# Kernel optimization log

Hardware: AMD Instinct MI355X
Metric: run time of the kernel (lower is better)

The kernel has to match this reference:

```python
import jax, jax.numpy as jnp
import numpy as np

B, R, DIM = 4096, 64, 128


def setup_inputs() -> dict:
    key = jax.random.key(0)
    ks = jax.random.split(key, 8)
    return {
        "query_emb": jax.random.normal(ks[0], (B, DIM), jnp.float32),
        "offset_emb": jax.random.normal(ks[1], (B, DIM), jnp.float32),
        "refer_embs": jax.random.normal(ks[2], (B, R, DIM), jnp.float32),
        "query_r": jax.random.normal(ks[3], (B, DIM), jnp.float32),
        "refer_r": jax.random.normal(ks[4], (B, R, DIM), jnp.float32),
        "start_embs": jax.random.normal(ks[5], (B, R, DIM), jnp.float32),
        # attn_layer_1: Linear(2*dim, dim); xavier-uniform-like scale
        "W1": jax.random.uniform(ks[6], (DIM, 2 * DIM), jnp.float32, -0.125, 0.125),
        "b1": jnp.zeros((DIM,), jnp.float32),
        # attn_layer_2: Linear(dim, dim)
        "W2": jax.random.uniform(ks[7], (DIM, DIM), jnp.float32, -0.125, 0.125),
        "b2": jnp.zeros((DIM,), jnp.float32),
    }


def reference(query_emb, offset_emb, refer_embs, query_r, refer_r, start_embs, W1, b1, W2, b2):
    # bias term per neighbor: [B, R, dim]
    bias = refer_embs - (start_embs + refer_r)
    # concat([refer_r, broadcast(query_r)]) @ W1.T split to avoid materializing the concat:
    # W1 = [W1_a | W1_b] over the 2*dim input axis
    W1a, W1b = W1[:, :DIM], W1[:, DIM:]
    h = jnp.einsum('brd,kd->brk', refer_r, W1a) \
        + jnp.einsum('bd,kd->bk', query_r, W1b)[:, None, :] + b1
    h = jax.nn.relu(h)  # [B, R, dim]
    attn = jnp.einsum('brk,dk->brd', h, W2) + b2  # attn_layer_2
    final_refer_emb = jnp.sum(attn * bias, axis=-2)  # [B, dim]
    final_query_emb = query_emb + final_refer_emb
    return (final_query_emb, offset_emb)
```

## Files before the change

### kernel.cpp

```cpp
#include <hip/hip_runtime.h>
#include <hip/hip_bf16.h>
#include <stdint.h>

#define BTOT 4096
#define RR   64
#define DIMD 128
#define WROW 40

typedef short s16x8 __attribute__((ext_vector_type(8)));
typedef float f32x4 __attribute__((ext_vector_type(4)));

__device__ __forceinline__ unsigned short f2bf(float x) {
  __hip_bfloat16 h = __float2bfloat16(x);
  return __builtin_bit_cast(unsigned short, h);
}
__device__ __forceinline__ float bf2f(unsigned short u) {
  unsigned int v = ((unsigned int)u) << 16;
  return __builtin_bit_cast(float, v);
}

__global__ __launch_bounds__(256) void prep_kernel(
    const float* __restrict__ W1, const float* __restrict__ b1,
    const float* __restrict__ query_r, const float* __restrict__ W2,
    const float* __restrict__ offset_emb,
    float* __restrict__ qproj, unsigned short* __restrict__ w1a_swz,
    unsigned short* __restrict__ w2_swz, float* __restrict__ out)
{
  __shared__ float w1b[128 * 132];
  __shared__ float qrs[256];
  const int tid = threadIdx.x;

  {
    const size_t ob = (size_t)blockIdx.x * 8 * DIMD + (size_t)tid * 4;
    *reinterpret_cast<float4*>(out + (size_t)BTOT * DIMD + ob) =
        *reinterpret_cast<const float4*>(offset_emb + ob);
  }
  {
    const int k = tid >> 1, d0 = (tid & 1) * 64;
    const float* src = W1 + k * 256 + 128 + d0;
    float* dst = &w1b[k * 132 + d0];
    #pragma unroll
    for (int i = 0; i < 64; i += 4)
      *reinterpret_cast<float4*>(dst + i) = *reinterpret_cast<const float4*>(src + i);
  }
  if (blockIdx.x < 2) {
    const float* Wsrc = (blockIdx.x == 0) ? W1 : W2;
    unsigned short* dstw = (blockIdx.x == 0) ? w1a_swz : w2_swz;
    const int stride = (blockIdx.x == 0) ? 256 : 128;
    for (int i = tid; i < 128 * 128; i += 256) {
      const int k = i >> 7, d = i & 127;
      dstw[k * 128 + (d ^ ((k & 7) << 3))] = f2bf(Wsrc[k * stride + d]);
    }
  }
  __syncthreads();

  const int b0 = blockIdx.x * 8;
  const int k = tid & 127, bh = tid >> 7;
  for (int p = 0; p < 4; ++p) {
    const int b = b0 + p * 2;
    qrs[tid] = query_r[(size_t)(b + bh) * DIMD + k];
    __syncthreads();
    float acc = b1[k];
    const float* qq = &qrs[bh * 128];
    const float* wr = &w1b[k * 132];
    #pragma unroll
    for (int d = 0; d < 128; d += 4) {
      float4 wv = *reinterpret_cast<const float4*>(wr + d);
      float4 qv = *reinterpret_cast<const float4*>(qq + d);
      acc = fmaf(wv.x, qv.x, acc); acc = fmaf(wv.y, qv.y, acc);
      acc = fmaf(wv.z, qv.z, acc); acc = fmaf(wv.w, qv.w, acc);
    }
    qproj[(size_t)(b + bh) * DIMD + k] = acc;
    __syncthreads();
  }
}

__global__ __launch_bounds__(512) void main_kernel(
    const float* __restrict__ query_emb,
    const float* __restrict__ refer_embs, const float* __restrict__ refer_r,
    const float* __restrict__ start_embs, const float* __restrict__ b2,
    const float* __restrict__ qproj, const unsigned short* __restrict__ w1a_swz,
    const unsigned short* __restrict__ w2_swz, float* __restrict__ out)
{
  __shared__ unsigned short lds_w1a[128 * 128];
  __shared__ unsigned short lds_w2[128 * 128];
  __shared__ unsigned short wbuf[8][16 * WROW];

  const int tid  = threadIdx.x;
  const int wave = tid >> 6;
  const int lane = tid & 63;
  const int g    = lane >> 4;
  const int c    = lane & 15;

  {
    const uint4* s1 = reinterpret_cast<const uint4*>(w1a_swz);
    const uint4* s2 = reinterpret_cast<const uint4*>(w2_swz);
    uint4* d1 = reinterpret_cast<uint4*>(lds_w1a);
    uint4* d2 = reinterpret_cast<uint4*>(lds_w2);
    #pragma unroll
    for (int i = 0; i < 4; ++i) {
      d1[tid + 512 * i] = s1[tid + 512 * i];
      d2[tid + 512 * i] = s2[tid + 512 * i];
    }
  }
  __syncthreads();

  unsigned short* mybuf = &wbuf[wave][0];
  const int srl = lane >> 2;
  const int q   = lane & 3;
  const int swc = (c & 7) << 3;
  const int rl4 = 4 * g;

  const int b = blockIdx.x * 8 + wave;

  float qn[8], b2v[8], acc[8];
  #pragma unroll
  for (int nt = 0; nt < 8; ++nt) {
    qn[nt]  = qproj[(size_t)b * DIMD + nt * 16 + c];
    b2v[nt] = b2[nt * 16 + c];
    acc[nt] = 0.f;
  }

  for (int it = 0; it < 4; ++it) {
    const size_t rowbase = ((size_t)b * RR + it * 16 + srl) * DIMD;
    uint4 bp[4];
    f32x4 Ch[8];
    #pragma unroll
    for (int nt = 0; nt < 8; ++nt) Ch[nt] = (f32x4){qn[nt], qn[nt], qn[nt], qn[nt]};

    #pragma unroll
    for (int Q = 0; Q < 4; ++Q) {
      const size_t gb = rowbase + Q * 32 + q * 8;
      const float4 rv0 = *reinterpret_cast<const float4*>(refer_r    + gb);
      const float4 rv1 = *reinterpret_cast<const float4*>(refer_r    + gb + 4);
      const float4 ev0 = *reinterpret_cast<const float4*>(refer_embs + gb);
      const float4 ev1 = *reinterpret_cast<const float4*>(refer_embs + gb + 4);
      const float4 sv0 = *reinterpret_cast<const float4*>(start_embs + gb);
      const float4 sv1 = *reinterpret_cast<const float4*>(start_embs + gb + 4);
      {
        union { unsigned short u[8]; uint4 v; } pk;
        pk.u[0] = f2bf(rv0.x); pk.u[1] = f2bf(rv0.y);
        pk.u[2] = f2bf(rv0.z); pk.u[3] = f2bf(rv0.w);
        pk.u[4] = f2bf(rv1.x); pk.u[5] = f2bf(rv1.y);
        pk.u[6] = f2bf(rv1.z); pk.u[7] = f2bf(rv1.w);
        *reinterpret_cast<uint4*>(&mybuf[srl * WROW + q * 8]) = pk.v;
      }
      {
        union { unsigned short u[8]; uint4 v; } pk;
        pk.u[0] = f2bf(ev0.x - sv0.x - rv0.x); pk.u[1] = f2bf(ev0.y - sv0.y - rv0.y);
        pk.u[2] = f2bf(ev0.z - sv0.z - rv0.z); pk.u[3] = f2bf(ev0.w - sv0.w - rv0.w);
        pk.u[4] = f2bf(ev1.x - sv1.x - rv1.x); pk.u[5] = f2bf(ev1.y - sv1.y - rv1.y);
        pk.u[6] = f2bf(ev1.z - sv1.z - rv1.z); pk.u[7] = f2bf(ev1.w - sv1.w - rv1.w);
        bp[Q] = pk.v;
      }
      asm volatile("s_waitcnt lgkmcnt(0)" ::: "memory");
      const s16x8 af = *reinterpret_cast<const s16x8*>(&mybuf[c * WROW + g * 8]);
      #pragma unroll
      for (int nt = 0; nt < 8; ++nt) {
        s16x8 wf = *reinterpret_cast<const s16x8*>(
            &lds_w1a[(nt * 16 + c) * DIMD + ((Q * 32 + g * 8) ^ swc)]);
        Ch[nt] = __builtin_amdgcn_mfma_f32_16x16x32_bf16(af, wf, Ch[nt], 0, 0, 0);
      }
      asm volatile("s_waitcnt lgkmcnt(0)" ::: "memory");
    }

    f32x4 Ca[8];
    #pragma unroll
    for (int nt = 0; nt < 8; ++nt) Ca[nt] = (f32x4){b2v[nt], b2v[nt], b2v[nt], b2v[nt]};
    #pragma unroll
    for (int Q = 0; Q < 4; ++Q) {
      #pragma unroll
      for (int ntl = 0; ntl < 2; ++ntl)
        #pragma unroll
        for (int r = 0; r < 4; ++r)
          mybuf[(rl4 + r) * WROW + ntl * 16 + c] = f2bf(fmaxf(Ch[2 * Q + ntl][r], 0.f));
      asm volatile("s_waitcnt lgkmcnt(0)" ::: "memory");
      const s16x8 hf = *reinterpret_cast<const s16x8*>(&mybuf[c * WROW + g * 8]);
      #pragma unroll
      for (int nt = 0; nt < 8; ++nt) {
        s16x8 wf = *reinterpret_cast<const s16x8*>(
            &lds_w2[(nt * 16 + c) * DIMD + ((Q * 32 + g * 8) ^ swc)]);
        Ca[nt] = __builtin_amdgcn_mfma_f32_16x16x32_bf16(hf, wf, Ca[nt], 0, 0, 0);
      }
      asm volatile("s_waitcnt lgkmcnt(0)" ::: "memory");
    }

    #pragma unroll
    for (int Q = 0; Q < 4; ++Q) {
      *reinterpret_cast<uint4*>(&mybuf[srl * WROW + q * 8]) = bp[Q];
      asm volatile("s_waitcnt lgkmcnt(0)" ::: "memory");
      #pragma unroll
      for (int ntl = 0; ntl < 2; ++ntl) {
        const int nt = 2 * Q + ntl;
        float s = 0.f;
        #pragma unroll
        for (int r = 0; r < 4; ++r) {
          const float bcv = bf2f(mybuf[(rl4 + r) * WROW + ntl * 16 + c]);
          s = fmaf(Ca[nt][r], bcv, s);
        }
        s += __shfl_xor(s, 16);
        s += __shfl_xor(s, 32);
        acc[nt] += s;
      }
      asm volatile("s_waitcnt lgkmcnt(0)" ::: "memory");
    }
  }

  if (lane < 16) {
    #pragma unroll
    for (int nt = 0; nt < 8; ++nt)
      out[(size_t)b * DIMD + nt * 16 + c] =
          query_emb[(size_t)b * DIMD + nt * 16 + c] + acc[nt];
  }
}

extern "C" void kernel_launch(void* const* d_in, const int* in_sizes, int n_in,
                              void* d_out, int out_size, void* d_ws, size_t ws_size,
                              hipStream_t stream) {
  const float* query_emb  = (const float*)d_in[0];
  const float* offset_emb = (const float*)d_in[1];
  const float* refer_embs = (const float*)d_in[2];
  const float* query_r    = (const float*)d_in[3];
  const float* refer_r    = (const float*)d_in[4];
  const float* start_embs = (const float*)d_in[5];
  const float* W1 = (const float*)d_in[6];
  const float* b1 = (const float*)d_in[7];
  const float* W2 = (const float*)d_in[8];
  const float* b2 = (const float*)d_in[9];
  float* out = (float*)d_out;

  float* qproj = (float*)d_ws;
  unsigned short* w1a_swz =
      (unsigned short*)((char*)d_ws + (size_t)BTOT * DIMD * sizeof(float));
  unsigned short* w2_swz = w1a_swz + 128 * 128;

  hipLaunchKernelGGL(prep_kernel, dim3(512), dim3(256), 0, stream,
                     W1, b1, query_r, W2, offset_emb, qproj, w1a_swz, w2_swz, out);
  hipLaunchKernelGGL(main_kernel, dim3(512), dim3(512), 0, stream,
                     query_emb, refer_embs, refer_r, start_embs,
                     b2, qproj, w1a_swz, w2_swz, out);
}
```

Baseline: 109.5 us.

## Process two batches per wave and prefetch next neighbor chunk loads

Each wave now handles two batch rows, with separate LDS staging buffers, and the grid is halved to 256 blocks. The global loads for the next 32-column chunk are issued before the current chunk's MFMAs, so memory latency overlaps with compute. The explicit s_waitcnt barriers are dropped, and LDS ordering is left to the compiler. This adds instruction-level parallelism and amortises the weight reads from LDS, at the cost of more registers and only one 8-wave block per CU, which lowers occupancy.

```diff
diff --git a/kernel.cpp b/kernel.cpp
--- a/kernel.cpp
+++ b/kernel.cpp
@@ -84,7 +84,7 @@
 {
   __shared__ unsigned short lds_w1a[128 * 128];
   __shared__ unsigned short lds_w2[128 * 128];
-  __shared__ unsigned short wbuf[8][16 * WROW];
+  __shared__ unsigned short tq[8][2][16 * WROW];
 
   const int tid  = threadIdx.x;
   const int wave = tid >> 6;
@@ -105,112 +105,158 @@
   }
   __syncthreads();
 
-  unsigned short* mybuf = &wbuf[wave][0];
   const int srl = lane >> 2;
   const int q   = lane & 3;
   const int swc = (c & 7) << 3;
   const int rl4 = 4 * g;
 
-  const int b = blockIdx.x * 8 + wave;
-
-  float qn[8], b2v[8], acc[8];
+  const int bA = blockIdx.x * 16 + wave * 2;
+  unsigned short* tch[2] = { &tq[wave][0][0], &tq[wave][1][0] };
+
+  float qn[2][8], acc[2][8], b2v[8];
   #pragma unroll
   for (int nt = 0; nt < 8; ++nt) {
-    qn[nt]  = qproj[(size_t)b * DIMD + nt * 16 + c];
     b2v[nt] = b2[nt * 16 + c];
-    acc[nt] = 0.f;
+    #pragma unroll
+    for (int j = 0; j < 2; ++j) {
+      qn[j][nt]  = qproj[(size_t)(bA + j) * DIMD + nt * 16 + c];
+      acc[j][nt] = 0.f;
+    }
   }
 
   for (int it = 0; it < 4; ++it) {
-    const size_t rowbase = ((size_t)b * RR + it * 16 + srl) * DIMD;
-    uint4 bp[4];
-    f32x4 Ch[8];
-    #pragma unroll
-    for (int nt = 0; nt < 8; ++nt) Ch[nt] = (f32x4){qn[nt], qn[nt], qn[nt], qn[nt]};
+    size_t rowbase[2];
+    #pragma unroll
+    for (int j = 0; j < 2; ++j)
+      rowbase[j] = ((size_t)(bA + j) * RR + it * 16 + srl) * DIMD;
+
+    float4 rv[2][2], ev[2][2], sv[2][2];
+    #pragma unroll
+    for (int j = 0; j < 2; ++j) {
+      const size_t gb = rowbase[j] + q * 8;
+      rv[j][0] = *reinterpret_cast<const float4*>(refer_r    + gb);
+      rv[j][1] = *reinterpret_cast<const float4*>(refer_r    + gb + 4);
+      ev[j][0] = *reinterpret_cast<const float4*>(refer_embs + gb);
+      ev[j][1] = *reinterpret_cast<const float4*>(refer_embs + gb + 4);
+      sv[j][0] = *reinterpret_cast<const float4*>(start_embs + gb);
+      sv[j][1] = *reinterpret_cast<const float4*>(start_embs + gb + 4);
+    }
+
+    uint4 bp[2][4];
+    f32x4 Ch[2][8];
+    #pragma unroll
+    for (int j = 0; j < 2; ++j)
+      #pragma unroll
+      for (int nt = 0; nt < 8; ++nt)
+        Ch[j][nt] = (f32x4){qn[j][nt], qn[j][nt], qn[j][nt], qn[j][nt]};
 
     #pragma unroll
     for (int Q = 0; Q < 4; ++Q) {
-      const size_t gb = rowbase + Q * 32 + q * 8;
-      const float4 rv0 = *reinterpret_cast<const float4*>(refer_r    + gb);
-      const float4 rv1 = *reinterpret_cast<const float4*>(refer_r    + gb + 4);
-      const float4 ev0 = *reinterpret_cast<const float4*>(refer_embs + gb);
-      const float4 ev1 = *reinterpret_cast<const float4*>(refer_embs + gb + 4);
-      const float4 sv0 = *reinterpret_cast<const float4*>(start_embs + gb);
-      const float4 sv1 = *reinterpret_cast<const float4*>(start_embs + gb + 4);
-      {
-        union { unsigned short u[8]; uint4 v; } pk;
-        pk.u[0] = f2bf(rv0.x); pk.u[1] = f2bf(rv0.y);
-        pk.u[2] = f2bf(rv0.z); pk.u[3] = f2bf(rv0.w);
-        pk.u[4] = f2bf(rv1.x); pk.u[5] = f2bf(rv1.y);
-        pk.u[6] = f2bf(rv1.z); pk.u[7] = f2bf(rv1.w);
-        *reinterpret_cast<uint4*>(&mybuf[srl * WROW + q * 8]) = pk.v;
-      }
-      {
-        union { unsigned short u[8]; uint4 v; } pk;
-        pk.u[0] = f2bf(ev0.x - sv0.x - rv0.x); pk.u[1] = f2bf(ev0.y - sv0.y - rv0.y);
-        pk.u[2] = f2bf(ev0.z - sv0.z - rv0.z); pk.u[3] = f2bf(ev0.w - sv0.w - rv0.w);
-        pk.u[4] = f2bf(ev1.x - sv1.x - rv1.x); pk.u[5] = f2bf(ev1.y - sv1.y - rv1.y);
-        pk.u[6] = f2bf(ev1.z - sv1.z - rv1.z); pk.u[7] = f2bf(ev1.w - sv1.w - rv1.w);
-        bp[Q] = pk.v;
-      }
-      asm volatile("s_waitcnt lgkmcnt(0)" ::: "memory");
-      const s16x8 af = *reinterpret_cast<const s16x8*>(&mybuf[c * WROW + g * 8]);
-      #pragma unroll
-      for (int nt = 0; nt < 8; ++nt) {
-        s16x8 wf = *reinterpret_cast<const s16x8*>(
-            &lds_w1a[(nt * 16 + c) * DIMD + ((Q * 32 + g * 8) ^ swc)]);
-        Ch[nt] = __builtin_amdgcn_mfma_f32_16x16x32_bf16(af, wf, Ch[nt], 0, 0, 0);
-      }
-      asm volatile("s_waitcnt lgkmcnt(0)" ::: "memory");
-    }
-
-    f32x4 Ca[8];
-    #pragma unroll
-    for (int nt = 0; nt < 8; ++nt) Ca[nt] = (f32x4){b2v[nt], b2v[nt], b2v[nt], b2v[nt]};
+      #pragma unroll
+      for (int j = 0; j < 2; ++j) {
+        {
+          union { unsigned short u[8]; uint4 v; } pk;
+          pk.u[0] = f2bf(rv[j][0].x); pk.u[1] = f2bf(rv[j][0].y);
+          pk.u[2] = f2bf(rv[j][0].z); pk.u[3] = f2bf(rv[j][0].w);
+          pk.u[4] = f2bf(rv[j][1].x); pk.u[5] = f2bf(rv[j][1].y);
+          pk.u[6] = f2bf(rv[j][1].z); pk.u[7] = f2bf(rv[j][1].w);
+          *reinterpret_cast<uint4*>(&tch[j][srl * WROW + q * 8]) = pk.v;
+        }
+        {
+          union { unsigned short u[8]; uint4 v; } pk;
+          pk.u[0] = f2bf(ev[j][0].x - sv[j][0].x - rv[j][0].x);
+          pk.u[1] = f2bf(ev[j][0].y - sv[j][0].y - rv[j][0].y);
+          pk.u[2] = f2bf(ev[j][0].z - sv[j][0].z - rv[j][0].z);
+          pk.u[3] = f2bf(ev[j][0].w - sv[j][0].w - rv[j][0].w);
+          pk.u[4] = f2bf(ev[j][1].x - sv[j][1].x - rv[j][1].x);
+          pk.u[5] = f2bf(ev[j][1].y - sv[j][1].y - rv[j][1].y);
+          pk.u[6] = f2bf(ev[j][1].z - sv[j][1].z - rv[j][1].z);
+          pk.u[7] = f2bf(ev[j][1].w - sv[j][1].w - rv[j][1].w);
+          bp[j][Q] = pk.v;
+        }
+      }
+      if (Q < 3) {
+        #pragma unroll
+        for (int j = 0; j < 2; ++j) {
+          const size_t gb = rowbase[j] + (Q + 1) * 32 + q * 8;
+          rv[j][0] = *reinterpret_cast<const float4*>(refer_r    + gb);
+          rv[j][1] = *reinterpret_cast<const float4*>(refer_r    + gb + 4);
+          ev[j][0] = *reinterpret_cast<const float4*>(refer_embs + gb);
+          ev[j][1] = *reinterpret_cast<const float4*>(refer_embs + gb + 4);
+          sv[j][0] = *reinterpret_cast<const float4*>(start_embs + gb);
+          sv[j][1] = *reinterpret_cast<const float4*>(start_embs + gb + 4);
+        }
+      }
+      #pragma unroll
+      for (int j = 0; j < 2; ++j) {
+        const s16x8 af = *reinterpret_cast<const s16x8*>(&tch[j][c * WROW + g * 8]);
+        #pragma unroll
+        for (int nt = 0; nt < 8; ++nt) {
+          s16x8 wf = *reinterpret_cast<const s16x8*>(
+              &lds_w1a[(nt * 16 + c) * DIMD + ((Q * 32 + g * 8) ^ swc)]);
+          Ch[j][nt] = __builtin_amdgcn_mfma_f32_16x16x32_bf16(af, wf, Ch[j][nt], 0, 0, 0);
+        }
+      }
+    }
+
+    f32x4 Ca[2][8];
+    #pragma unroll
+    for (int j = 0; j < 2; ++j)
+      #pragma unroll
+      for (int nt = 0; nt < 8; ++nt)
+        Ca[j][nt] = (f32x4){b2v[nt], b2v[nt], b2v[nt], b2v[nt]};
     #pragma unroll
     for (int Q = 0; Q < 4; ++Q) {
       #pragma unroll
-      for (int ntl = 0; ntl < 2; ++ntl)
-        #pragma unroll
-        for (int r = 0; r < 4; ++r)
-          mybuf[(rl4 + r) * WROW + ntl * 16 + c] = f2bf(fmaxf(Ch[2 * Q + ntl][r], 0.f));
-      asm volatile("s_waitcnt lgkmcnt(0)" ::: "memory");
-      const s16x8 hf = *reinterpret_cast<const s16x8*>(&mybuf[c * WROW + g * 8]);
-      #pragma unroll
-      for (int nt = 0; nt < 8; ++nt) {
-        s16x8 wf = *reinterpret_cast<const s16x8*>(
-            &lds_w2[(nt * 16 + c) * DIMD + ((Q * 32 + g * 8) ^ swc)]);
-        Ca[nt] = __builtin_amdgcn_mfma_f32_16x16x32_bf16(hf, wf, Ca[nt], 0, 0, 0);
-      }
-      asm volatile("s_waitcnt lgkmcnt(0)" ::: "memory");
+      for (int j = 0; j < 2; ++j)
+        #pragma unroll
+        for (int ntl = 0; ntl < 2; ++ntl)
+          #pragma unroll
+          for (int r = 0; r < 4; ++r)
+            tch[j][(rl4 + r) * WROW + ntl * 16 + c] =
+                f2bf(fmaxf(Ch[j][2 * Q + ntl][r], 0.f));
+      #pragma unroll
+      for (int j = 0; j < 2; ++j) {
+        const s16x8 hf = *reinterpret_cast<const s16x8*>(&tch[j][c * WROW + g * 8]);
+        #pragma unroll
+        for (int nt = 0; nt < 8; ++nt) {
+          s16x8 wf = *reinterpret_cast<const s16x8*>(
+              &lds_w2[(nt * 16 + c) * DIMD + ((Q * 32 + g * 8) ^ swc)]);
+          Ca[j][nt] = __builtin_amdgcn_mfma_f32_16x16x32_bf16(hf, wf, Ca[j][nt], 0, 0, 0);
+        }
+      }
     }
 
     #pragma unroll
     for (int Q = 0; Q < 4; ++Q) {
-      *reinterpret_cast<uint4*>(&mybuf[srl * WROW + q * 8]) = bp[Q];
-      asm volatile("s_waitcnt lgkmcnt(0)" ::: "memory");
-      #pragma unroll
-      for (int ntl = 0; ntl < 2; ++ntl) {
-        const int nt = 2 * Q + ntl;
-        float s = 0.f;
-        #pragma unroll
-        for (int r = 0; r < 4; ++r) {
-          const float bcv = bf2f(mybuf[(rl4 + r) * WROW + ntl * 16 + c]);
-          s = fmaf(Ca[nt][r], bcv, s);
-        }
-        s += __shfl_xor(s, 16);
-        s += __shfl_xor(s, 32);
-        acc[nt] += s;
-      }
-      asm volatile("s_waitcnt lgkmcnt(0)" ::: "memory");
+      #pragma unroll
+      for (int j = 0; j < 2; ++j)
+        *reinterpret_cast<uint4*>(&tch[j][srl * WROW + q * 8]) = bp[j][Q];
+      #pragma unroll
+      for (int j = 0; j < 2; ++j)
+        #pragma unroll
+        for (int ntl = 0; ntl < 2; ++ntl) {
+          const int nt = 2 * Q + ntl;
+          float s = 0.f;
+          #pragma unroll
+          for (int r = 0; r < 4; ++r) {
+            const float bcv = bf2f(tch[j][(rl4 + r) * WROW + ntl * 16 + c]);
+            s = fmaf(Ca[j][nt][r], bcv, s);
+          }
+          s += __shfl_xor(s, 16);
+          s += __shfl_xor(s, 32);
+          acc[j][nt] += s;
+        }
     }
   }
 
   if (lane < 16) {
     #pragma unroll
-    for (int nt = 0; nt < 8; ++nt)
-      out[(size_t)b * DIMD + nt * 16 + c] =
-          query_emb[(size_t)b * DIMD + nt * 16 + c] + acc[nt];
+    for (int j = 0; j < 2; ++j)
+      #pragma unroll
+      for (int nt = 0; nt < 8; ++nt)
+        out[(size_t)(bA + j) * DIMD + nt * 16 + c] =
+            query_emb[(size_t)(bA + j) * DIMD + nt * 16 + c] + acc[j][nt];
   }
 }
 
@@ -236,7 +282,7 @@
 
   hipLaunchKernelGGL(prep_kernel, dim3(512), dim3(256), 0, stream,
                      W1, b1, query_r, W2, offset_emb, qproj, w1a_swz, w2_swz, out);
-  hipLaunchKernelGGL(main_kernel, dim3(512), dim3(512), 0, stream,
+  hipLaunchKernelGGL(main_kernel, dim3(256), dim3(512), 0, stream,
                      query_emb, refer_embs, refer_r, start_embs,
                      b2, qproj, w1a_swz, w2_swz, out);
 }
```

After: 151.9 us. 1.39x slower.

## Prefetch next neighbor chunk into registers and process two batches per wave

Applied to the files above, without the earlier changes.

Each wave now handles two batch rows, and the grid shrinks to 256 blocks, so the LDS weight staging is amortized over more work. The global loads of refer_r, refer_embs and start_embs for the next 32-column chunk are issued before the current chunk's MFMAs run, forming a register double-buffer across the whole two-batch sequence. The explicit lgkmcnt waits are removed and left to the compiler. The goal is to hide HBM latency in this memory-bound kernel, at the cost of more live registers and fewer resident waves per CU.

```diff
diff --git a/kernel.cpp b/kernel.cpp
--- a/kernel.cpp
+++ b/kernel.cpp
@@ -111,107 +111,125 @@
   const int swc = (c & 7) << 3;
   const int rl4 = 4 * g;
 
-  const int b = blockIdx.x * 8 + wave;
-
-  float qn[8], b2v[8], acc[8];
+  const int bA = blockIdx.x * 16 + wave * 2;
+
+  float b2v[8];
   #pragma unroll
-  for (int nt = 0; nt < 8; ++nt) {
-    qn[nt]  = qproj[(size_t)b * DIMD + nt * 16 + c];
-    b2v[nt] = b2[nt * 16 + c];
-    acc[nt] = 0.f;
-  }
-
-  for (int it = 0; it < 4; ++it) {
-    const size_t rowbase = ((size_t)b * RR + it * 16 + srl) * DIMD;
-    uint4 bp[4];
-    f32x4 Ch[8];
-    #pragma unroll
-    for (int nt = 0; nt < 8; ++nt) Ch[nt] = (f32x4){qn[nt], qn[nt], qn[nt], qn[nt]};
-
-    #pragma unroll
-    for (int Q = 0; Q < 4; ++Q) {
-      const size_t gb = rowbase + Q * 32 + q * 8;
-      const float4 rv0 = *reinterpret_cast<const float4*>(refer_r    + gb);
-      const float4 rv1 = *reinterpret_cast<const float4*>(refer_r    + gb + 4);
-      const float4 ev0 = *reinterpret_cast<const float4*>(refer_embs + gb);
-      const float4 ev1 = *reinterpret_cast<const float4*>(refer_embs + gb + 4);
-      const float4 sv0 = *reinterpret_cast<const float4*>(start_embs + gb);
-      const float4 sv1 = *reinterpret_cast<const float4*>(start_embs + gb + 4);
-      {
-        union { unsigned short u[8]; uint4 v; } pk;
-        pk.u[0] = f2bf(rv0.x); pk.u[1] = f2bf(rv0.y);
-        pk.u[2] = f2bf(rv0.z); pk.u[3] = f2bf(rv0.w);
-        pk.u[4] = f2bf(rv1.x); pk.u[5] = f2bf(rv1.y);
-        pk.u[6] = f2bf(rv1.z); pk.u[7] = f2bf(rv1.w);
-        *reinterpret_cast<uint4*>(&mybuf[srl * WROW + q * 8]) = pk.v;
+  for (int nt = 0; nt < 8; ++nt) b2v[nt] = b2[nt * 16 + c];
+
+  float4 Prv0, Prv1, Pev0, Pev1, Psv0, Psv1;
+
+#define LOADQ(fq) do {                                                        \
+    const int bb_ = (fq) >> 4, it_ = ((fq) >> 2) & 3, Q_ = (fq) & 3;          \
+    const size_t gb_ =                                                        \
+        ((size_t)(bA + bb_) * RR + it_ * 16 + srl) * DIMD + Q_ * 32 + q * 8;  \
+    Prv0 = *reinterpret_cast<const float4*>(refer_r    + gb_);                \
+    Prv1 = *reinterpret_cast<const float4*>(refer_r    + gb_ + 4);            \
+    Pev0 = *reinterpret_cast<const float4*>(refer_embs + gb_);                \
+    Pev1 = *reinterpret_cast<const float4*>(refer_embs + gb_ + 4);            \
+    Psv0 = *reinterpret_cast<const float4*>(start_embs + gb_);                \
+    Psv1 = *reinterpret_cast<const float4*>(start_embs + gb_ + 4);            \
+  } while (0)
+
+  LOADQ(0);
+
+  #pragma unroll
+  for (int bb = 0; bb < 2; ++bb) {
+    const int b = bA + bb;
+
+    float qn[8], acc[8];
+    #pragma unroll
+    for (int nt = 0; nt < 8; ++nt) {
+      qn[nt]  = qproj[(size_t)b * DIMD + nt * 16 + c];
+      acc[nt] = 0.f;
+    }
+
+    for (int it = 0; it < 4; ++it) {
+      uint4 bp[4];
+      f32x4 Ch[8];
+      #pragma unroll
+      for (int nt = 0; nt < 8; ++nt) Ch[nt] = (f32x4){qn[nt], qn[nt], qn[nt], qn[nt]};
+
+      #pragma unroll
+      for (int Q = 0; Q < 4; ++Q) {
+        {
+          union { unsigned short u[8]; uint4 v; } pk;
+          pk.u[0] = f2bf(Prv0.x); pk.u[1] = f2bf(Prv0.y);
+          pk.u[2] = f2bf(Prv0.z); pk.u[3] = f2bf(Prv0.w);
+          pk.u[4] = f2bf(Prv1.x); pk.u[5] = f2bf(Prv1.y);
+          pk.u[6] = f2bf(Prv1.z); pk.u[7] = f2bf(Prv1.w);
+          *reinterpret_cast<uint4*>(&mybuf[srl * WROW + q * 8]) = pk.v;
+        }
+        {
+          union { unsigned short u[8]; uint4 v; } pk;
+          pk.u[0] = f2bf(Pev0.x - Psv0.x - Prv0.x);
+          pk.u[1] = f2bf(Pev0.y - Psv0.y - Prv0.y);
+          pk.u[2] = f2bf(Pev0.z - Psv0.z - Prv0.z);
+          pk.u[3] = f2bf(Pev0.w - Psv0.w - Prv0.w);
+          pk.u[4] = f2bf(Pev1.x - Psv1.x - Prv1.x);
+          pk.u[5] = f2bf(Pev1.y - Psv1.y - Prv1.y);
+          pk.u[6] = f2bf(Pev1.z - Psv1.z - Prv1.z);
+          pk.u[7] = f2bf(Pev1.w - Psv1.w - Prv1.w);
+          bp[Q] = pk.v;
+        }
+        const int fq = bb * 16 + it * 4 + Q;
+        if (fq + 1 < 32) { LOADQ(fq + 1); }
+        const s16x8 af = *reinterpret_cast<const s16x8*>(&mybuf[c * WROW + g * 8]);
+        #pragma unroll
+        for (int nt = 0; nt < 8; ++nt) {
+          s16x8 wf = *reinterpret_cast<const s16x8*>(
+              &lds_w1a[(nt * 16 + c) * DIMD + ((Q * 32 + g * 8) ^ swc)]);
+          Ch[nt] = __builtin_amdgcn_mfma_f32_16x16x32_bf16(af, wf, Ch[nt], 0, 0, 0);
+        }
       }
-      {
-        union { unsigned short u[8]; uint4 v; } pk;
-        pk.u[0] = f2bf(ev0.x - sv0.x - rv0.x); pk.u[1] = f2bf(ev0.y - sv0.y - rv0.y);
-        pk.u[2] = f2bf(ev0.z - sv0.z - rv0.z); pk.u[3] = f2bf(ev0.w - sv0.w - rv0.w);
-        pk.u[4] = f2bf(ev1.x - sv1.x - rv1.x); pk.u[5] = f2bf(ev1.y - sv1.y - rv1.y);
-        pk.u[6] = f2bf(ev1.z - sv1.z - rv1.z); pk.u[7] = f2bf(ev1.w - sv1.w - rv1.w);
-        bp[Q] = pk.v;
+
+      f32x4 Ca[8];
+      #pragma unroll
+      for (int nt = 0; nt < 8; ++nt) Ca[nt] = (f32x4){b2v[nt], b2v[nt], b2v[nt], b2v[nt]};
+      #pragma unroll
+      for (int Q = 0; Q < 4; ++Q) {
+        #pragma unroll
+        for (int ntl = 0; ntl < 2; ++ntl)
+          #pragma unroll
+          for (int r = 0; r < 4; ++r)
+            mybuf[(rl4 + r) * WROW + ntl * 16 + c] =
+                f2bf(fmaxf(Ch[2 * Q + ntl][r], 0.f));
+        const s16x8 hf = *reinterpret_cast<const s16x8*>(&mybuf[c * WROW + g * 8]);
+        #pragma unroll
+        for (int nt = 0; nt < 8; ++nt) {
+          s16x8 wf = *reinterpret_cast<const s16x8*>(
+              &lds_w2[(nt * 16 + c) * DIMD + ((Q * 32 + g * 8) ^ swc)]);
+          Ca[nt] = __builtin_amdgcn_mfma_f32_16x16x32_bf16(hf, wf, Ca[nt], 0, 0, 0);
+        }
       }
-      asm volatile("s_waitcnt lgkmcnt(0)" ::: "memory");
-      const s16x8 af = *reinterpret_cast<const s16x8*>(&mybuf[c * WROW + g * 8]);
-      #pragma unroll
-      for (int nt = 0; nt < 8; ++nt) {
-        s16x8 wf = *reinterpret_cast<const s16x8*>(
-            &lds_w1a[(nt * 16 + c) * DIMD + ((Q * 32 + g * 8) ^ swc)]);
-        Ch[nt] = __builtin_amdgcn_mfma_f32_16x16x32_bf16(af, wf, Ch[nt], 0, 0, 0);
+
+      #pragma unroll
+      for (int Q = 0; Q < 4; ++Q) {
+        *reinterpret_cast<uint4*>(&mybuf[srl * WROW + q * 8]) = bp[Q];
+        #pragma unroll
+        for (int ntl = 0; ntl < 2; ++ntl) {
+          const int nt = 2 * Q + ntl;
+          float s = 0.f;
+          #pragma unroll
+          for (int r = 0; r < 4; ++r) {
+            const float bcv = bf2f(mybuf[(rl4 + r) * WROW + ntl * 16 + c]);
+            s = fmaf(Ca[nt][r], bcv, s);
+          }
+          s += __shfl_xor(s, 16);
+          s += __shfl_xor(s, 32);
+          acc[nt] += s;
+        }
       }
-      asm volatile("s_waitcnt lgkmcnt(0)" ::: "memory");
-    }
-
-    f32x4 Ca[8];
-    #pragma unroll
-    for (int nt = 0; nt < 8; ++nt) Ca[nt] = (f32x4){b2v[nt], b2v[nt], b2v[nt], b2v[nt]};
-    #pragma unroll
-    for (int Q = 0; Q < 4; ++Q) {
-      #pragma unroll
-      for (int ntl = 0; ntl < 2; ++ntl)
-        #pragma unroll
-        for (int r = 0; r < 4; ++r)
-          mybuf[(rl4 + r) * WROW + ntl * 16 + c] = f2bf(fmaxf(Ch[2 * Q + ntl][r], 0.f));
-      asm volatile("s_waitcnt lgkmcnt(0)" ::: "memory");
-      const s16x8 hf = *reinterpret_cast<const s16x8*>(&mybuf[c * WROW + g * 8]);
-      #pragma unroll
-      for (int nt = 0; nt < 8; ++nt) {
-        s16x8 wf = *reinterpret_cast<const s16x8*>(
-            &lds_w2[(nt * 16 + c) * DIMD + ((Q * 32 + g * 8) ^ swc)]);
-        Ca[nt] = __builtin_amdgcn_mfma_f32_16x16x32_bf16(hf, wf, Ca[nt], 0, 0, 0);
-      }
-      asm volatile("s_waitcnt lgkmcnt(0)" ::: "memory");
-    }
-
-    #pragma unroll
-    for (int Q = 0; Q < 4; ++Q) {
-      *reinterpret_cast<uint4*>(&mybuf[srl * WROW + q * 8]) = bp[Q];
-      asm volatile("s_waitcnt lgkmcnt(0)" ::: "memory");
-      #pragma unroll
-      for (int ntl = 0; ntl < 2; ++ntl) {
-        const int nt = 2 * Q + ntl;
-        float s = 0.f;
-        #pragma unroll
-        for (int r = 0; r < 4; ++r) {
-          const float bcv = bf2f(mybuf[(rl4 + r) * WROW + ntl * 16 + c]);
-          s = fmaf(Ca[nt][r], bcv, s);
-        }
-        s += __shfl_xor(s, 16);
-        s += __shfl_xor(s, 32);
-        acc[nt] += s;
-      }
-      asm volatile("s_waitcnt lgkmcnt(0)" ::: "memory");
-    }
-  }
-
-  if (lane < 16) {
-    #pragma unroll
-    for (int nt = 0; nt < 8; ++nt)
-      out[(size_t)b * DIMD + nt * 16 + c] =
-          query_emb[(size_t)b * DIMD + nt * 16 + c] + acc[nt];
-  }
+    }
+
+    if (lane < 16) {
+      #pragma unroll
+      for (int nt = 0; nt < 8; ++nt)
+        out[(size_t)b * DIMD + nt * 16 + c] =
+            query_emb[(size_t)b * DIMD + nt * 16 + c] + acc[nt];
+    }
+  }
+#undef LOADQ
 }
 
 extern "C" void kernel_launch(void* const* d_in, const int* in_sizes, int n_in,
@@ -236,7 +254,7 @@
 
   hipLaunchKernelGGL(prep_kernel, dim3(512), dim3(256), 0, stream,
                      W1, b1, query_r, W2, offset_emb, qproj, w1a_swz, w2_swz, out);
-  hipLaunchKernelGGL(main_kernel, dim3(512), dim3(512), 0, stream,
+  hipLaunchKernelGGL(main_kernel, dim3(256), dim3(512), 0, stream,
                      query_emb, refer_embs, refer_r, start_embs,
                      b2, qproj, w1a_swz, w2_swz, out);
 }
```

After: 174.3 us. 1.59x slower.

## Keep MFMA operands in registers via transposed product and permuted weight columns

Applied to the files above, without the earlier changes.

Swaps the MFMA operand order so each lane computes a transposed output tile. Together with a K-permutation baked into the preprocessed weight layout, the activations loaded from global memory, the ReLU hidden values and the bias term can then feed the next MFMA straight from registers, with no round trip through a per-wave LDS staging buffer. This removes LDS stores and loads and the waitcnt barriers between stages. Accumulation now happens per lane, followed by one cross-lane shuffle reduction at the end. Global loads become 16-byte strided per row rather than 32-byte contiguous chunks, and register pressure rises because whole rows are held in registers.

```diff
diff --git a/kernel.cpp b/kernel.cpp
--- a/kernel.cpp
+++ b/kernel.cpp
@@ -5,7 +5,6 @@
 #define BTOT 4096
 #define RR   64
 #define DIMD 128
-#define WROW 40
 
 typedef short s16x8 __attribute__((ext_vector_type(8)));
 typedef float f32x4 __attribute__((ext_vector_type(4)));
@@ -14,17 +13,22 @@
   __hip_bfloat16 h = __float2bfloat16(x);
   return __builtin_bit_cast(unsigned short, h);
 }
-__device__ __forceinline__ float bf2f(unsigned short u) {
-  unsigned int v = ((unsigned int)u) << 16;
-  return __builtin_bit_cast(float, v);
+__device__ __forceinline__ unsigned int pk2(float lo, float hi) {
+  return ((unsigned int)f2bf(hi) << 16) | (unsigned int)f2bf(lo);
+}
+__device__ __forceinline__ float bflo(unsigned int u) {
+  return __builtin_bit_cast(float, u << 16);
+}
+__device__ __forceinline__ float bfhi(unsigned int u) {
+  return __builtin_bit_cast(float, u & 0xFFFF0000u);
 }
 
 __global__ __launch_bounds__(256) void prep_kernel(
     const float* __restrict__ W1, const float* __restrict__ b1,
     const float* __restrict__ query_r, const float* __restrict__ W2,
     const float* __restrict__ offset_emb,
-    float* __restrict__ qproj, unsigned short* __restrict__ w1a_swz,
-    unsigned short* __restrict__ w2_swz, float* __restrict__ out)
+    float* __restrict__ qproj, unsigned short* __restrict__ w1a_t,
+    unsigned short* __restrict__ w2_t, float* __restrict__ out)
 {
   __shared__ float w1b[128 * 132];
   __shared__ float qrs[256];
@@ -45,11 +49,12 @@
   }
   if (blockIdx.x < 2) {
     const float* Wsrc = (blockIdx.x == 0) ? W1 : W2;
-    unsigned short* dstw = (blockIdx.x == 0) ? w1a_swz : w2_swz;
+    unsigned short* dstw = (blockIdx.x == 0) ? w1a_t : w2_t;
     const int stride = (blockIdx.x == 0) ? 256 : 128;
     for (int i = tid; i < 128 * 128; i += 256) {
-      const int k = i >> 7, d = i & 127;
-      dstw[k * 128 + (d ^ ((k & 7) << 3))] = f2bf(Wsrc[k * stride + d]);
+      const int k = i >> 7, s = i & 127;
+      const int d = 32 * (s >> 5) + 16 * ((s >> 2) & 1) + 4 * ((s >> 3) & 3) + (s & 3);
+      dstw[k * 128 + (s ^ ((k & 7) << 3))] = f2bf(Wsrc[k * stride + d]);
     }
   }
   __syncthreads();
@@ -79,12 +84,11 @@
     const float* __restrict__ query_emb,
     const float* __restrict__ refer_embs, const float* __restrict__ refer_r,
     const float* __restrict__ start_embs, const float* __restrict__ b2,
-    const float* __restrict__ qproj, const unsigned short* __restrict__ w1a_swz,
-    const unsigned short* __restrict__ w2_swz, float* __restrict__ out)
+    const float* __restrict__ qproj, const unsigned short* __restrict__ w1a_t,
+    const unsigned short* __restrict__ w2_t, float* __restrict__ out)
 {
   __shared__ unsigned short lds_w1a[128 * 128];
   __shared__ unsigned short lds_w2[128 * 128];
-  __shared__ unsigned short wbuf[8][16 * WROW];
 
   const int tid  = threadIdx.x;
   const int wave = tid >> 6;
@@ -93,8 +97,8 @@
   const int c    = lane & 15;
 
   {
-    const uint4* s1 = reinterpret_cast<const uint4*>(w1a_swz);
-    const uint4* s2 = reinterpret_cast<const uint4*>(w2_swz);
+    const uint4* s1 = reinterpret_cast<const uint4*>(w1a_t);
+    const uint4* s2 = reinterpret_cast<const uint4*>(w2_t);
     uint4* d1 = reinterpret_cast<uint4*>(lds_w1a);
     uint4* d2 = reinterpret_cast<uint4*>(lds_w2);
     #pragma unroll
@@ -105,112 +109,103 @@
   }
   __syncthreads();
 
-  unsigned short* mybuf = &wbuf[wave][0];
-  const int srl = lane >> 2;
-  const int q   = lane & 3;
   const int swc = (c & 7) << 3;
-  const int rl4 = 4 * g;
-
   const int b = blockIdx.x * 8 + wave;
 
-  float qn[8], b2v[8], acc[8];
+  f32x4 acc[8];
   #pragma unroll
-  for (int nt = 0; nt < 8; ++nt) {
-    qn[nt]  = qproj[(size_t)b * DIMD + nt * 16 + c];
-    b2v[nt] = b2[nt * 16 + c];
-    acc[nt] = 0.f;
-  }
+  for (int nt = 0; nt < 8; ++nt) acc[nt] = (f32x4){0.f, 0.f, 0.f, 0.f};
+
+  union U16x8 { unsigned int u[4]; s16x8 v; };
 
   for (int it = 0; it < 4; ++it) {
-    const size_t rowbase = ((size_t)b * RR + it * 16 + srl) * DIMD;
-    uint4 bp[4];
+    const size_t rowoff = ((size_t)b * RR + it * 16 + c) * DIMD + 4 * g;
+    const float* rp = refer_r    + rowoff;
+    const float* ep = refer_embs + rowoff;
+    const float* sp = start_embs + rowoff;
+
+    unsigned int rrpk[16], bp[16];
+    #pragma unroll
+    for (int nt = 0; nt < 8; ++nt) {
+      const float4 rv = *reinterpret_cast<const float4*>(rp + 16 * nt);
+      const float4 ev = *reinterpret_cast<const float4*>(ep + 16 * nt);
+      const float4 sv = *reinterpret_cast<const float4*>(sp + 16 * nt);
+      rrpk[2 * nt + 0] = pk2(rv.x, rv.y);
+      rrpk[2 * nt + 1] = pk2(rv.z, rv.w);
+      bp[2 * nt + 0] = pk2(ev.x - sv.x - rv.x, ev.y - sv.y - rv.y);
+      bp[2 * nt + 1] = pk2(ev.z - sv.z - rv.z, ev.w - sv.w - rv.w);
+    }
+
     f32x4 Ch[8];
     #pragma unroll
-    for (int nt = 0; nt < 8; ++nt) Ch[nt] = (f32x4){qn[nt], qn[nt], qn[nt], qn[nt]};
-
-    #pragma unroll
-    for (int Q = 0; Q < 4; ++Q) {
-      const size_t gb = rowbase + Q * 32 + q * 8;
-      const float4 rv0 = *reinterpret_cast<const float4*>(refer_r    + gb);
-      const float4 rv1 = *reinterpret_cast<const float4*>(refer_r    + gb + 4);
-      const float4 ev0 = *reinterpret_cast<const float4*>(refer_embs + gb);
-      const float4 ev1 = *reinterpret_cast<const float4*>(refer_embs + gb + 4);
-      const float4 sv0 = *reinterpret_cast<const float4*>(start_embs + gb);
-      const float4 sv1 = *reinterpret_cast<const float4*>(start_embs + gb + 4);
-      {
-        union { unsigned short u[8]; uint4 v; } pk;
-        pk.u[0] = f2bf(rv0.x); pk.u[1] = f2bf(rv0.y);
-        pk.u[2] = f2bf(rv0.z); pk.u[3] = f2bf(rv0.w);
-        pk.u[4] = f2bf(rv1.x); pk.u[5] = f2bf(rv1.y);
-        pk.u[6] = f2bf(rv1.z); pk.u[7] = f2bf(rv1.w);
-        *reinterpret_cast<uint4*>(&mybuf[srl * WROW + q * 8]) = pk.v;
-      }
-      {
-        union { unsigned short u[8]; uint4 v; } pk;
-        pk.u[0] = f2bf(ev0.x - sv0.x - rv0.x); pk.u[1] = f2bf(ev0.y - sv0.y - rv0.y);
-        pk.u[2] = f2bf(ev0.z - sv0.z - rv0.z); pk.u[3] = f2bf(ev0.w - sv0.w - rv0.w);
-        pk.u[4] = f2bf(ev1.x - sv1.x - rv1.x); pk.u[5] = f2bf(ev1.y - sv1.y - rv1.y);
-        pk.u[6] = f2bf(ev1.z - sv1.z - rv1.z); pk.u[7] = f2bf(ev1.w - sv1.w - rv1.w);
-        bp[Q] = pk.v;
-      }
-      asm volatile("s_waitcnt lgkmcnt(0)" ::: "memory");
-      const s16x8 af = *reinterpret_cast<const s16x8*>(&mybuf[c * WROW + g * 8]);
+    for (int nt = 0; nt < 8; ++nt)
+      Ch[nt] = *reinterpret_cast<const f32x4*>(qproj + (size_t)b * DIMD + 16 * nt + 4 * g);
+    #pragma unroll
+    for (int ck = 0; ck < 4; ++ck) {
+      U16x8 af;
+      af.u[0] = rrpk[4 * ck + 0]; af.u[1] = rrpk[4 * ck + 1];
+      af.u[2] = rrpk[4 * ck + 2]; af.u[3] = rrpk[4 * ck + 3];
       #pragma unroll
       for (int nt = 0; nt < 8; ++nt) {
         s16x8 wf = *reinterpret_cast<const s16x8*>(
-            &lds_w1a[(nt * 16 + c) * DIMD + ((Q * 32 + g * 8) ^ swc)]);
-        Ch[nt] = __builtin_amdgcn_mfma_f32_16x16x32_bf16(af, wf, Ch[nt], 0, 0, 0);
+            &lds_w1a[(nt * 16 + c) * DIMD + ((ck * 32 + g * 8) ^ swc)]);
+        Ch[nt] = __builtin_amdgcn_mfma_f32_16x16x32_bf16(wf, af.v, Ch[nt], 0, 0, 0);
       }
-      asm volatile("s_waitcnt lgkmcnt(0)" ::: "memory");
+    }
+
+    unsigned int hpk[16];
+    #pragma unroll
+    for (int nt = 0; nt < 8; ++nt) {
+      hpk[2 * nt + 0] = pk2(fmaxf(Ch[nt][0], 0.f), fmaxf(Ch[nt][1], 0.f));
+      hpk[2 * nt + 1] = pk2(fmaxf(Ch[nt][2], 0.f), fmaxf(Ch[nt][3], 0.f));
     }
 
     f32x4 Ca[8];
     #pragma unroll
-    for (int nt = 0; nt < 8; ++nt) Ca[nt] = (f32x4){b2v[nt], b2v[nt], b2v[nt], b2v[nt]};
-    #pragma unroll
-    for (int Q = 0; Q < 4; ++Q) {
-      #pragma unroll
-      for (int ntl = 0; ntl < 2; ++ntl)
-        #pragma unroll
-        for (int r = 0; r < 4; ++r)
-          mybuf[(rl4 + r) * WROW + ntl * 16 + c] = f2bf(fmaxf(Ch[2 * Q + ntl][r], 0.f));
-      asm volatile("s_waitcnt lgkmcnt(0)" ::: "memory");
-      const s16x8 hf = *reinterpret_cast<const s16x8*>(&mybuf[c * WROW + g * 8]);
+    for (int nt = 0; nt < 8; ++nt)
+      Ca[nt] = *reinterpret_cast<const f32x4*>(b2 + 16 * nt + 4 * g);
+    #pragma unroll
+    for (int ck = 0; ck < 4; ++ck) {
+      U16x8 hf;
+      hf.u[0] = hpk[4 * ck + 0]; hf.u[1] = hpk[4 * ck + 1];
+      hf.u[2] = hpk[4 * ck + 2]; hf.u[3] = hpk[4 * ck + 3];
       #pragma unroll
       for (int nt = 0; nt < 8; ++nt) {
         s16x8 wf = *reinterpret_cast<const s16x8*>(
-            &lds_w2[(nt * 16 + c) * DIMD + ((Q * 32 + g * 8) ^ swc)]);
-        Ca[nt] = __builtin_amdgcn_mfma_f32_16x16x32_bf16(hf, wf, Ca[nt], 0, 0, 0);
+            &lds_w2[(nt * 16 + c) * DIMD + ((ck * 32 + g * 8) ^ swc)]);
+        Ca[nt] = __builtin_amdgcn_mfma_f32_16x16x32_bf16(wf, hf.v, Ca[nt], 0, 0, 0);
       }
-      asm volatile("s_waitcnt lgkmcnt(0)" ::: "memory");
-    }
-
-    #pragma unroll
-    for (int Q = 0; Q < 4; ++Q) {
-      *reinterpret_cast<uint4*>(&mybuf[srl * WROW + q * 8]) = bp[Q];
-      asm volatile("s_waitcnt lgkmcnt(0)" ::: "memory");
-      #pragma unroll
-      for (int ntl = 0; ntl < 2; ++ntl) {
-        const int nt = 2 * Q + ntl;
-        float s = 0.f;
-        #pragma unroll
-        for (int r = 0; r < 4; ++r) {
-          const float bcv = bf2f(mybuf[(rl4 + r) * WROW + ntl * 16 + c]);
-          s = fmaf(Ca[nt][r], bcv, s);
-        }
-        s += __shfl_xor(s, 16);
-        s += __shfl_xor(s, 32);
-        acc[nt] += s;
-      }
-      asm volatile("s_waitcnt lgkmcnt(0)" ::: "memory");
-    }
-  }
-
-  if (lane < 16) {
-    #pragma unroll
-    for (int nt = 0; nt < 8; ++nt)
-      out[(size_t)b * DIMD + nt * 16 + c] =
-          query_emb[(size_t)b * DIMD + nt * 16 + c] + acc[nt];
+    }
+
+    #pragma unroll
+    for (int nt = 0; nt < 8; ++nt) {
+      acc[nt][0] = fmaf(Ca[nt][0], bflo(bp[2 * nt + 0]), acc[nt][0]);
+      acc[nt][1] = fmaf(Ca[nt][1], bfhi(bp[2 * nt + 0]), acc[nt][1]);
+      acc[nt][2] = fmaf(Ca[nt][2], bflo(bp[2 * nt + 1]), acc[nt][2]);
+      acc[nt][3] = fmaf(Ca[nt][3], bfhi(bp[2 * nt + 1]), acc[nt][3]);
+    }
+  }
+
+  #pragma unroll
+  for (int mask = 1; mask <= 8; mask <<= 1)
+    #pragma unroll
+    for (int nt = 0; nt < 8; ++nt) {
+      acc[nt][0] += __shfl_xor(acc[nt][0], mask);
+      acc[nt][1] += __shfl_xor(acc[nt][1], mask);
+      acc[nt][2] += __shfl_xor(acc[nt][2], mask);
+      acc[nt][3] += __shfl_xor(acc[nt][3], mask);
+    }
+
+  if (c == 0) {
+    #pragma unroll
+    for (int nt = 0; nt < 8; ++nt) {
+      const size_t o = (size_t)b * DIMD + 16 * nt + 4 * g;
+      const float4 qe = *reinterpret_cast<const float4*>(query_emb + o);
+      float4 r;
+      r.x = qe.x + acc[nt][0]; r.y = qe.y + acc[nt][1];
+      r.z = qe.z + acc[nt][2]; r.w = qe.w + acc[nt][3];
+      *reinterpret_cast<float4*>(out + o) = r;
+    }
   }
 }
 
@@ -230,13 +225,13 @@
   float* out = (float*)d_out;
 
   float* qproj = (float*)d_ws;
-  unsigned short* w1a_swz =
+  unsigned short* w1a_t =
       (unsigned short*)((char*)d_ws + (size_t)BTOT * DIMD * sizeof(float));
-  unsigned short* w2_swz = w1a_swz + 128 * 128;
+  unsigned short* w2_t = w1a_t + 128 * 128;
 
   hipLaunchKernelGGL(prep_kernel, dim3(512), dim3(256), 0, stream,
-                     W1, b1, query_r, W2, offset_emb, qproj, w1a_swz, w2_swz, out);
+                     W1, b1, query_r, W2, offset_emb, qproj, w1a_t, w2_t, out);
   hipLaunchKernelGGL(main_kernel, dim3(512), dim3(512), 0, stream,
                      query_emb, refer_embs, refer_r, start_embs,
-                     b2, qproj, w1a_swz, w2_swz, out);
-}
+                     b2, qproj, w1a_t, w2_t, out);
+}
```

After: 258.1 us. 2.36x slower.
